# Kernel tuning notes

Hardware: AMD Instinct MI355X
Metric: run time of the kernel (lower is better)

The kernel has to match this reference:

```python
import jax, jax.numpy as jnp
import numpy as np

N_NODES = 10000
N_EDGES = 320000
N_GRAPHS = 64
K = 10
IN_C, HID_C, OUT_C = 128, 256, 128


def setup_inputs() -> dict:
    key = jax.random.key(0)
    ks = jax.random.split(key, 10)
    s_in = 1.0 / np.sqrt(IN_C)
    s_hid = 1.0 / np.sqrt(HID_C)
    return {
        "x": jax.random.normal(ks[0], (N_NODES, IN_C), jnp.float32),
        "W0": jax.random.normal(ks[1], (K, IN_C, HID_C), jnp.float32) * s_in,
        "b0": jnp.zeros((HID_C,), jnp.float32),
        "W1": jax.random.normal(ks[2], (K, HID_C, HID_C), jnp.float32) * s_hid,
        "b1": jnp.zeros((HID_C,), jnp.float32),
        "W2": jax.random.normal(ks[3], (K, HID_C, HID_C), jnp.float32) * s_hid,
        "b2": jnp.zeros((HID_C,), jnp.float32),
        "W_out": jax.random.normal(ks[4], (HID_C, OUT_C), jnp.float32) * s_hid,
        "b_out": jnp.zeros((OUT_C,), jnp.float32),
        "edge_index": jax.random.randint(ks[5], (2, N_EDGES), 0, N_NODES, jnp.int64),
        "batch": jnp.sort(jax.random.randint(ks[6], (N_NODES,), 0, N_GRAPHS, jnp.int64)),
    }


def _edge_norm(src, dst, n):
    # Scaled Laplacian L_hat = 2L/lambda_max - I with lambda_max=2 and sym norm
    # => L_hat = -D^{-1/2} A D^{-1/2} (diagonal entries cancel to 0).
    deg = jnp.zeros((n,), jnp.float32).at[src].add(1.0)
    dis = jnp.where(deg > 0, jax.lax.rsqrt(jnp.maximum(deg, 1.0)), 0.0)
    return -dis[src] * dis[dst]


def _propagate(x, src, dst, w, n):
    # message = w * x[src], aggregated by sum at dst
    return jax.ops.segment_sum(w[:, None] * x[src], dst, num_segments=n)


def _cheb_conv(x, src, dst, w, W, b, n):
    # Tx_0 = x; Tx_1 = L_hat x; Tx_k = 2 L_hat Tx_{k-1} - Tx_{k-2}
    K_ = W.shape[0]
    Tx0 = x
    out = Tx0 @ W[0]
    Tx1 = _propagate(Tx0, src, dst, w, n)
    out = out + Tx1 @ W[1]
    for k in range(2, K_):
        Tx2 = 2.0 * _propagate(Tx1, src, dst, w, n) - Tx0
        out = out + Tx2 @ W[k]
        Tx0, Tx1 = Tx1, Tx2
    return out + b


def reference(x, W0, b0, W1, b1, W2, b2, W_out, b_out, edge_index, batch):
    n = x.shape[0]
    src, dst = edge_index[0], edge_index[1]
    w = _edge_norm(src, dst, n)
    # 3 ChebConv layers, each followed by ReLU (norm=None, dropout=0)
    h = jax.nn.relu(_cheb_conv(x, src, dst, w, W0, b0, n))
    h = jax.nn.relu(_cheb_conv(h, src, dst, w, W1, b1, n))
    h = jax.nn.relu(_cheb_conv(h, src, dst, w, W2, b2, n))
    # global_mean_pool over batch ids
    sums = jax.ops.segment_sum(h, batch, num_segments=N_GRAPHS)
    cnts = jax.ops.segment_sum(jnp.ones((n,), h.dtype), batch, num_segments=N_GRAPHS)
    pooled = sums / jnp.maximum(cnts, 1.0)[:, None]
    return pooled @ W_out + b_out
```

## Files before the change

### kernel.cpp

```cpp
#include <hip/hip_runtime.h>
#include <cstdint>
#include <cstddef>

#define N_NODES 10000
#define N_EDGES 320000
#define N_GRAPHS 64
#define KCHEB 10
#define C_IN 128
#define C_HID 256
#define C_OUTC 128
#define POOL_CHUNK 40

static inline size_t align_up(size_t v, size_t a){ return (v + a - 1) / a * a; }

typedef __attribute__((ext_vector_type(8))) _Float16 half8;
typedef __attribute__((ext_vector_type(2))) _Float16 h2;
typedef __attribute__((ext_vector_type(4))) float f32x4;


__global__ void k_deg(const int* __restrict__ src, const int* __restrict__ dst,
                      int* __restrict__ deg, int* __restrict__ indeg){
  int e = blockIdx.x*blockDim.x + threadIdx.x;
  if(e < N_EDGES){
    atomicAdd(&deg[src[e]], 1);
    atomicAdd(&indeg[dst[e]], 1);
  }
}

__global__ __launch_bounds__(1024) void k_scan(const int* __restrict__ cnt,
                                               int* __restrict__ offs,
                                               int* __restrict__ cursor,
                                               const int* __restrict__ deg,
                                               float* __restrict__ dis,
                                               int* __restrict__ perm){
  __shared__ int part[1024];
  __shared__ int hist[256];
  __shared__ int hoff[256];
  const int n = N_NODES;
  const int CH = (n + 1023) / 1024;
  int tid = threadIdx.x;
  int base = tid * CH;
  if(tid < 256) hist[tid] = 0;
  int s = 0;
  for(int i = 0; i < CH; i++){
    int idx = base + i;
    if(idx < n){
      s += cnt[idx];
      int d = deg[idx];
      dis[idx] = d > 0 ? rsqrtf((float)d) : 0.f;
    }
  }
  part[tid] = s;
  __syncthreads();
  for(int off = 1; off < 1024; off <<= 1){
    int v = (tid >= off) ? part[tid - off] : 0;
    __syncthreads();
    part[tid] += v;
    __syncthreads();
  }
  int run = (tid == 0) ? 0 : part[tid - 1];
  for(int i = 0; i < CH; i++){
    int idx = base + i;
    if(idx < n){
      offs[idx] = run;
      cursor[idx] = run;
      run += cnt[idx];
      int d = cnt[idx]; if(d > 255) d = 255;
      atomicAdd(&hist[d], 1);
    }
  }
  if(tid == 1023) offs[n] = part[1023];
  __syncthreads();
  if(tid == 0){
    int r2 = 0;
    for(int d = 255; d >= 0; d--){ hoff[d] = r2; r2 += hist[d]; }
  }
  __syncthreads();
  for(int i = 0; i < CH; i++){
    int idx = base + i;
    if(idx < n){
      int d = cnt[idx]; if(d > 255) d = 255;
      int p0 = atomicAdd(&hoff[d], 1);
      perm[p0] = idx;
    }
  }
}

__global__ void k_scatter(const int* __restrict__ src, const int* __restrict__ dst,
                          const float* __restrict__ dis, int* __restrict__ cursor,
                          int* __restrict__ csr_s, unsigned* __restrict__ csr_wp){
  int e = blockIdx.x*blockDim.x + threadIdx.x;
  if(e < N_EDGES){
    int s = src[e], d = dst[e];
    float w = -dis[s] * dis[d];
    unsigned short wb = __builtin_bit_cast(unsigned short, (_Float16)w);
    int p = atomicAdd(&cursor[d], 1);
    csr_s[p] = s;
    csr_wp[p] = (unsigned)wb * 0x00010001u;
  }
}

__global__ __launch_bounds__(128) void k_gbounds(const int* __restrict__ batch,
                                                 int* __restrict__ gstart,
                                                 int* __restrict__ gcnt){
  int g = threadIdx.x;
  if(g <= N_GRAPHS){
    int lo = 0, hi = N_NODES;
    while(lo < hi){
      int mid = (lo + hi) >> 1;
      if(batch[mid] < g) lo = mid + 1; else hi = mid;
    }
    gstart[g] = lo;
  }
  __syncthreads();
  if(g < N_GRAPHS) gcnt[g] = gstart[g + 1] - gstart[g];
}


__device__ inline void hfma4(h2* a, uint4 v, unsigned wbits){
  h2 w2 = __builtin_bit_cast(h2, wbits);
  a[0] += __builtin_bit_cast(h2, v.x) * w2;
  a[1] += __builtin_bit_cast(h2, v.y) * w2;
  a[2] += __builtin_bit_cast(h2, v.z) * w2;
  a[3] += __builtin_bit_cast(h2, v.w) * w2;
}

__global__ __launch_bounds__(256) void k_prop256h(const _Float16* __restrict__ Xb,
                                                  const _Float16* __restrict__ Pb,
                                                  _Float16* __restrict__ tx,
                                                  const int* __restrict__ csr_s,
                                                  const unsigned* __restrict__ csr_wp,
                                                  const int* __restrict__ offs,
                                                  const int* __restrict__ perm,
                                                  float alpha){
  const int stride  = KCHEB * C_HID;
  const int strideB = stride * 2;
  int bid  = blockIdx.x;
  int half = (bid >> 2) & 1;
  int lh   = (bid >> 3) * 4 + (bid & 3);
  int l15  = threadIdx.x & 15;
  int lane = threadIdx.x & 63;
  int b16  = lane & 48;
  int e8   = l15 & 7;
  int nidx = lh * 16 + (threadIdx.x >> 4);
  if(nidx >= N_NODES) return;
  int node = perm[nidx];
  int j0 = offs[node], j1 = offs[node + 1];
  h2 a[4] = {};
  const char* __restrict__ gbase = (const char*)Xb + (half * (C_HID/2) + l15 * 8) * 2;
  int j = j0;
  int sv = 0; unsigned wv = 0;
  bool have = (j + 7 < j1);
  if(have){ sv = csr_s[j + e8] * strideB; wv = csr_wp[j + e8]; }
  while(have){
    int jn = j + 8;
    bool more = (jn + 7 < j1);
    int sv2 = 0; unsigned wv2 = 0;
    if(more){ sv2 = csr_s[jn + e8] * strideB; wv2 = csr_wp[jn + e8]; }
    uint4 v[8];
#pragma unroll
    for(int i = 0; i < 8; i++){
      int si = __shfl(sv, b16 + i);
      v[i] = *(const uint4*)(gbase + si);
    }
#pragma unroll
    for(int i = 0; i < 8; i++){
      unsigned wi = (unsigned)__shfl((int)wv, b16 + i);
      hfma4(a, v[i], wi);
    }
    sv = sv2; wv = wv2; j = jn; have = more;
  }
  for(; j < j1; j++){
    int si = csr_s[j] * strideB;
    uint4 v0 = *(const uint4*)(gbase + si);
    hfma4(a, v0, csr_wp[j]);
  }
  _Float16 ah = (_Float16)alpha;
  h2 al = {ah, ah};
  h2 r[4];
#pragma unroll
  for(int i = 0; i < 4; i++) r[i] = a[i] * al;
  size_t off = (size_t)node * stride + half * (C_HID/2) + l15 * 8;
  if(Pb){
    uint4 pv = *(const uint4*)(Pb + off);
    r[0] -= __builtin_bit_cast(h2, pv.x);
    r[1] -= __builtin_bit_cast(h2, pv.y);
    r[2] -= __builtin_bit_cast(h2, pv.z);
    r[3] -= __builtin_bit_cast(h2, pv.w);
  }
  uint4 ob;
  ob.x = __builtin_bit_cast(unsigned, r[0]);
  ob.y = __builtin_bit_cast(unsigned, r[1]);
  ob.z = __builtin_bit_cast(unsigned, r[2]);
  ob.w = __builtin_bit_cast(unsigned, r[3]);
  *(uint4*)(tx + off) = ob;
}

__global__ __launch_bounds__(256) void k_prop128(const _Float16* __restrict__ Xb,
                                                 const _Float16* __restrict__ Pb,
                                                 _Float16* __restrict__ tx,
                                                 const int* __restrict__ csr_s,
                                                 const unsigned* __restrict__ csr_wp,
                                                 const int* __restrict__ offs,
                                                 const int* __restrict__ perm,
                                                 float alpha){
  const int stride  = KCHEB * C_IN;
  const int strideB = stride * 2;
  int hl   = threadIdx.x & 31;
  int b32  = threadIdx.x & 32;
  int e8   = hl & 7;
  int node = perm[blockIdx.x * 8 + (threadIdx.x >> 5)];
  int j0 = offs[node], j1 = offs[node + 1];
  h2 a[2] = {};
  const char* __restrict__ gbase = (const char*)Xb + hl * 8;
  int j = j0;
  int sv = 0; unsigned wv = 0;
  bool have = (j + 7 < j1);
  if(have){ sv = csr_s[j + e8] * strideB; wv = csr_wp[j + e8]; }
  while(have){
    int jn = j + 8;
    bool more = (jn + 7 < j1);
    int sv2 = 0; unsigned wv2 = 0;
    if(more){ sv2 = csr_s[jn + e8] * strideB; wv2 = csr_wp[jn + e8]; }
    uint2 v[8];
#pragma unroll
    for(int i = 0; i < 8; i++){
      int si = __shfl(sv, b32 + i);
      v[i] = *(const uint2*)(gbase + si);
    }
#pragma unroll
    for(int i = 0; i < 8; i++){
      unsigned wi = (unsigned)__shfl((int)wv, b32 + i);
      h2 w2 = __builtin_bit_cast(h2, wi);
      a[0] += __builtin_bit_cast(h2, v[i].x) * w2;
      a[1] += __builtin_bit_cast(h2, v[i].y) * w2;
    }
    sv = sv2; wv = wv2; j = jn; have = more;
  }
  for(; j < j1; j++){
    int si = csr_s[j] * strideB;
    h2 w2 = __builtin_bit_cast(h2, csr_wp[j]);
    uint2 v0 = *(const uint2*)(gbase + si);
    a[0] += __builtin_bit_cast(h2, v0.x) * w2;
    a[1] += __builtin_bit_cast(h2, v0.y) * w2;
  }
  _Float16 ah = (_Float16)alpha;
  h2 al = {ah, ah};
  h2 r0 = a[0] * al, r1 = a[1] * al;
  size_t off = (size_t)node * stride + hl * 4;
  if(Pb){
    uint2 pv = *(const uint2*)(Pb + off);
    r0 -= __builtin_bit_cast(h2, pv.x);
    r1 -= __builtin_bit_cast(h2, pv.y);
  }
  uint2 ob;
  ob.x = __builtin_bit_cast(unsigned, r0);
  ob.y = __builtin_bit_cast(unsigned, r1);
  *(uint2*)(tx + off) = ob;
}

template<int C>
__global__ void k_f2h(const float* __restrict__ X, _Float16* __restrict__ tx,
                      int tx_stride){
  int idx = blockIdx.x * blockDim.x + threadIdx.x;
  const int GPR = C / 4;
  if(idx < N_NODES * GPR){
    int r = idx / GPR;
    int c = (idx - r * GPR) * 4;
    float4 v = *(const float4*)(X + (size_t)r * C + c);
    h2 p0 = {(_Float16)v.x, (_Float16)v.y};
    h2 p1 = {(_Float16)v.z, (_Float16)v.w};
    uint2 ob;
    ob.x = __builtin_bit_cast(unsigned, p0);
    ob.y = __builtin_bit_cast(unsigned, p1);
    *(uint2*)(tx + (size_t)r * tx_stride + c) = ob;
  }
}

__global__ __launch_bounds__(256) void k_wt3t(const float* __restrict__ W0, _Float16* __restrict__ WT0,
                                              const float* __restrict__ W1, _Float16* __restrict__ WT1,
                                              const float* __restrict__ W2, _Float16* __restrict__ WT2){
  __shared__ float t[32][33];
  int b = blockIdx.x;
  const float* W; _Float16* WT; int R; int tb;
  if(b < 320){ W = W0; WT = WT0; R = 1280; tb = b; }
  else if(b < 960){ W = W1; WT = WT1; R = 2560; tb = b - 320; }
  else { W = W2; WT = WT2; R = 2560; tb = b - 960; }
  int tr = tb >> 3, tc = tb & 7;
  int tx = threadIdx.x & 31, ty = threadIdx.x >> 5;
#pragma unroll
  for(int i = 0; i < 4; i++){
    int r = tr * 32 + ty + 8 * i;
    t[ty + 8 * i][tx] = W[(size_t)r * 256 + tc * 32 + tx];
  }
  __syncthreads();
#pragma unroll
  for(int i = 0; i < 4; i++){
    int o = tc * 32 + ty + 8 * i;
    WT[(size_t)o * R + tr * 32 + tx] = (_Float16)t[tx][ty + 8 * i];
  }
}


__global__ __launch_bounds__(256) void k_gemm_f(const _Float16* __restrict__ A,
                                                const _Float16* __restrict__ BT,
                                                const float* __restrict__ bias,
                                                float* __restrict__ H,
                                                _Float16* __restrict__ tx2,
                                                int M, int Ktot){
  int b = blockIdx.x;
  int xcd = b & 7;
  int l = b >> 3;
  int m = xcd + 8 * (l >> 2);
  int n = l & 3;
  if(m * 64 >= M) return;
  int row0 = m * 64, col0 = n * 64;

  __shared__ short As[2][64 * 64];
  __shared__ short Bs[2][64 * 64];
  int tid = threadIdx.x;
  int lane = tid & 63;
  int wave = tid >> 6;
  int l15 = lane & 15;
  int quad = lane >> 4;
  int wm = (wave & 1) * 32;
  int wn = (wave >> 1) * 32;

  int e0 = tid, e1 = tid + 256;
  int r0 = e0 >> 3, g0 = e0 & 7;
  int r1 = e1 >> 3, g1 = e1 & 7;
  int gr0 = row0 + r0, gr1 = row0 + r1;
  int sa0 = r0 * 64 + ((g0 ^ (r0 & 7)) * 8);
  int sa1 = r1 * 64 + ((g1 ^ (r1 & 7)) * 8);

  f32x4 acc[2][2] = {};
  uint4 av0, av1, bv0, bv1;

  auto load = [&](int k0){
    av0 = (gr0 < M) ? *(const uint4*)(A + (size_t)gr0 * Ktot + k0 + g0 * 8)
                    : make_uint4(0u, 0u, 0u, 0u);
    av1 = (gr1 < M) ? *(const uint4*)(A + (size_t)gr1 * Ktot + k0 + g1 * 8)
                    : make_uint4(0u, 0u, 0u, 0u);
    bv0 = *(const uint4*)(BT + (size_t)(col0 + r0) * Ktot + k0 + g0 * 8);
    bv1 = *(const uint4*)(BT + (size_t)(col0 + r1) * Ktot + k0 + g1 * 8);
  };
  auto stor = [&](int buf){
    *(uint4*)(&As[buf][sa0]) = av0;
    *(uint4*)(&As[buf][sa1]) = av1;
    *(uint4*)(&Bs[buf][sa0]) = bv0;
    *(uint4*)(&Bs[buf][sa1]) = bv1;
  };

  load(0);
  stor(0);
  __syncthreads();
  int nk = Ktot >> 6;
  for(int it = 0; it < nk; it++){
    int cur = it & 1;
    if(it + 1 < nk) load((it + 1) << 6);
#pragma unroll
    for(int kk = 0; kk < 64; kk += 32){
      int g = (kk >> 3) + quad;
      half8 a[2], bb[2];
#pragma unroll
      for(int mi = 0; mi < 2; mi++){
        int r = wm + mi * 16 + l15;
        a[mi] = *(const half8*)(&As[cur][r * 64 + ((g ^ (r & 7)) * 8)]);
      }
#pragma unroll
      for(int ni = 0; ni < 2; ni++){
        int nn = wn + ni * 16 + l15;
        bb[ni] = *(const half8*)(&Bs[cur][nn * 64 + ((g ^ (nn & 7)) * 8)]);
      }
#pragma unroll
      for(int mi = 0; mi < 2; mi++)
#pragma unroll
        for(int ni = 0; ni < 2; ni++)
          acc[mi][ni] = __builtin_amdgcn_mfma_f32_16x16x32_f16(a[mi], bb[ni], acc[mi][ni], 0, 0, 0);
    }
    if(it + 1 < nk){
      stor(cur ^ 1);
      __syncthreads();
    }
  }

  const int K256 = KCHEB * C_HID;
#pragma unroll
  for(int mi = 0; mi < 2; mi++){
#pragma unroll
    for(int ni = 0; ni < 2; ni++){
      int gcol = col0 + wn + ni * 16 + l15;
      float bv = bias[gcol];
#pragma unroll
      for(int r = 0; r < 4; r++){
        int grow = row0 + wm + mi * 16 + quad * 4 + r;
        if(grow < M){
          float v = fmaxf(acc[mi][ni][r] + bv, 0.f);
          if(tx2) tx2[(size_t)grow * K256 + gcol] = (_Float16)v;
          else    H[(size_t)grow * C_HID + gcol] = v;
        }
      }
    }
  }
}


__global__ __launch_bounds__(256) void k_pool2(const float* __restrict__ h,
                                               const int* __restrict__ batch,
                                               float* __restrict__ gsum){
  int c  = threadIdx.x;
  int n0 = blockIdx.x * POOL_CHUNK;
  int n1 = n0 + POOL_CHUNK;
  if(n1 > N_NODES) n1 = N_NODES;
  if(n0 >= n1) return;
  float acc = 0.f;
  int cur = batch[n0];
  for(int n = n0; n < n1; n++){
    int g = batch[n];
    if(g != cur){
      atomicAdd(&gsum[cur * C_HID + c], acc);
      acc = 0.f;
      cur = g;
    }
    acc += h[(size_t)n * C_HID + c];
  }
  atomicAdd(&gsum[cur * C_HID + c], acc);
}

__global__ __launch_bounds__(128) void k_final(const float* __restrict__ gsum,
                                               const int* __restrict__ gcnt,
                                               const float* __restrict__ Wout,
                                               const float* __restrict__ bout,
                                               float* __restrict__ out){
  int g = blockIdx.x;
  int o = threadIdx.x;
  float inv = 1.f / fmaxf((float)gcnt[g], 1.f);
  float acc = bout[o];
  for(int c = 0; c < C_HID; c++) acc += gsum[g * C_HID + c] * inv * Wout[c * C_OUTC + o];
  out[g * C_OUTC + o] = acc;
}


extern "C" void kernel_launch(void* const* d_in, const int* in_sizes, int n_in,
                              void* d_out, int out_size, void* d_ws, size_t ws_size,
                              hipStream_t stream){
  const float* x    = (const float*)d_in[0];
  const float* W0   = (const float*)d_in[1];
  const float* b0   = (const float*)d_in[2];
  const float* W1   = (const float*)d_in[3];
  const float* b1   = (const float*)d_in[4];
  const float* W2   = (const float*)d_in[5];
  const float* b2   = (const float*)d_in[6];
  const float* Wout = (const float*)d_in[7];
  const float* bout = (const float*)d_in[8];
  const int*   ei   = (const int*)d_in[9];
  const int*   batch= (const int*)d_in[10];
  const int* src = ei;
  const int* dst = ei + N_EDGES;
  float* out = (float*)d_out;

  char* p = (char*)d_ws;
  auto alloc = [&](size_t bytes)->char*{ char* r = p; p += align_up(bytes, 256); return r; };

  int*   deg    = (int*)  alloc(N_NODES * 4);
  int*   indeg  = (int*)  alloc(N_NODES * 4);
  int*   offs   = (int*)  alloc((N_NODES + 1) * 4);
  int*   cursor = (int*)  alloc(N_NODES * 4);
  float* dis    = (float*)alloc(N_NODES * 4);
  int*   perm   = (int*)  alloc(N_NODES * 4);
  int*   csr_s  = (int*)  alloc(N_EDGES * 4);
  unsigned* csr_wp = (unsigned*)alloc(N_EDGES * 4);
  int*   gcnt   = (int*)  alloc(N_GRAPHS * 4);
  int*   gstart = (int*)  alloc((N_GRAPHS + 1) * 4);
  float* gsum   = (float*)alloc(N_GRAPHS * C_HID * 4);

  const size_t txBytes = (size_t)N_NODES * (KCHEB * C_HID) * 2;
  _Float16* txP = (_Float16*)alloc(txBytes);
  _Float16* txQ = (_Float16*)alloc(txBytes);
  _Float16* WT0 = (_Float16*)alloc((size_t)KCHEB * C_IN  * C_HID * 2);
  _Float16* WT1 = (_Float16*)alloc((size_t)KCHEB * C_HID * C_HID * 2);
  _Float16* WT2 = (_Float16*)alloc((size_t)KCHEB * C_HID * C_HID * 2);
  float* Hb = (float*)alloc((size_t)N_NODES * C_HID * 4);

  hipMemsetAsync(deg,   0, N_NODES * 4, stream);
  hipMemsetAsync(indeg, 0, N_NODES * 4, stream);
  hipMemsetAsync(gsum,  0, N_GRAPHS * C_HID * 4, stream);

  const int TB = 256;
  int egrid = (N_EDGES + TB - 1) / TB;

  k_deg<<<egrid, TB, 0, stream>>>(src, dst, deg, indeg);
  k_scan<<<1, 1024, 0, stream>>>(indeg, offs, cursor, deg, dis, perm);
  k_scatter<<<egrid, TB, 0, stream>>>(src, dst, dis, cursor, csr_s, csr_wp);
  k_gbounds<<<1, 128, 0, stream>>>(batch, gstart, gcnt);
  k_wt3t<<<1600, 256, 0, stream>>>(W0, WT0, W1, WT1, W2, WT2);

  const int K128 = KCHEB * C_IN;
  const int K256 = KCHEB * C_HID;
  const int GEMM_BLOCKS = 640;
  const int PROP_H_BLOCKS = 1256;
  const int PROP_1_BLOCKS = N_NODES / 8;

  {
    int ng = N_NODES * (C_IN / 4);
    k_f2h<C_IN><<<(ng + TB - 1) / TB, TB, 0, stream>>>(x, txP, K128);
    for(int k = 1; k < KCHEB; k++){
      const _Float16* Xb = txP + (size_t)(k - 1) * C_IN;
      const _Float16* Pb = (k >= 2) ? txP + (size_t)(k - 2) * C_IN : nullptr;
      _Float16* tx = txP + (size_t)k * C_IN;
      k_prop128<<<PROP_1_BLOCKS, 256, 0, stream>>>(Xb, Pb, tx, csr_s, csr_wp, offs, perm,
                                                   k == 1 ? 1.f : 2.f);
    }
    k_gemm_f<<<GEMM_BLOCKS, 256, 0, stream>>>(txP, WT0, b0, nullptr, txQ, N_NODES, K128);
  }

  {
    for(int k = 1; k < KCHEB; k++){
      const _Float16* Xb = txQ + (size_t)(k - 1) * C_HID;
      const _Float16* Pb = (k >= 2) ? txQ + (size_t)(k - 2) * C_HID : nullptr;
      _Float16* tx = txQ + (size_t)k * C_HID;
      k_prop256h<<<PROP_H_BLOCKS, 256, 0, stream>>>(Xb, Pb, tx, csr_s, csr_wp, offs, perm,
                                                    k == 1 ? 1.f : 2.f);
    }
    k_gemm_f<<<GEMM_BLOCKS, 256, 0, stream>>>(txQ, WT1, b1, nullptr, txP, N_NODES, K256);
  }

  {
    for(int k = 1; k < KCHEB; k++){
      const _Float16* Xb = txP + (size_t)(k - 1) * C_HID;
      const _Float16* Pb = (k >= 2) ? txP + (size_t)(k - 2) * C_HID : nullptr;
      _Float16* tx = txP + (size_t)k * C_HID;
      k_prop256h<<<PROP_H_BLOCKS, 256, 0, stream>>>(Xb, Pb, tx, csr_s, csr_wp, offs, perm,
                                                    k == 1 ? 1.f : 2.f);
    }
    k_gemm_f<<<GEMM_BLOCKS, 256, 0, stream>>>(txP, WT2, b2, Hb, nullptr, N_NODES, K256);
  }

  k_pool2<<<(N_NODES + POOL_CHUNK - 1) / POOL_CHUNK, 256, 0, stream>>>(Hb, batch, gsum);
  k_final<<<N_GRAPHS, C_OUTC, 0, stream>>>(gsum, gcnt, Wout, bout, out);
}
```

Measured before the change: 626.8 us.

## Fuse mean-pool into last GEMM epilogue and merge small setup kernels

The final GEMM now stages its ReLU output tile in shared memory and accumulates per-graph column sums directly with atomics. This removes the fp32 H buffer write/read and the separate pooling kernel. Graph-boundary search moves into the scan kernel, and the x-to-half conversion is merged into the weight transpose kernel, cutting launch count. Atomic contention per GEMM block may increase slightly.

```diff
diff --git a/kernel.cpp b/kernel.cpp
--- a/kernel.cpp
+++ b/kernel.cpp
@@ -9,7 +9,6 @@
 #define C_IN 128
 #define C_HID 256
 #define C_OUTC 128
-#define POOL_CHUNK 40
 
 static inline size_t align_up(size_t v, size_t a){ return (v + a - 1) / a * a; }
 
@@ -32,7 +31,10 @@
                                                int* __restrict__ cursor,
                                                const int* __restrict__ deg,
                                                float* __restrict__ dis,
-                                               int* __restrict__ perm){
+                                               int* __restrict__ perm,
+                                               const int* __restrict__ batch,
+                                               int* __restrict__ gstart,
+                                               int* __restrict__ gcnt){
   __shared__ int part[1024];
   __shared__ int hist[256];
   __shared__ int hoff[256];
@@ -41,6 +43,14 @@
   int tid = threadIdx.x;
   int base = tid * CH;
   if(tid < 256) hist[tid] = 0;
+  if(tid <= N_GRAPHS){
+    int lo = 0, hi = N_NODES;
+    while(lo < hi){
+      int mid = (lo + hi) >> 1;
+      if(batch[mid] < tid) lo = mid + 1; else hi = mid;
+    }
+    gstart[tid] = lo;
+  }
   int s = 0;
   for(int i = 0; i < CH; i++){
     int idx = base + i;
@@ -52,6 +62,7 @@
   }
   part[tid] = s;
   __syncthreads();
+  if(tid < N_GRAPHS) gcnt[tid] = gstart[tid + 1] - gstart[tid];
   for(int off = 1; off < 1024; off <<= 1){
     int v = (tid >= off) ? part[tid - off] : 0;
     __syncthreads();
@@ -98,22 +109,6 @@
     csr_s[p] = s;
     csr_wp[p] = (unsigned)wb * 0x00010001u;
   }
-}
-
-__global__ __launch_bounds__(128) void k_gbounds(const int* __restrict__ batch,
-                                                 int* __restrict__ gstart,
-                                                 int* __restrict__ gcnt){
-  int g = threadIdx.x;
-  if(g <= N_GRAPHS){
-    int lo = 0, hi = N_NODES;
-    while(lo < hi){
-      int mid = (lo + hi) >> 1;
-      if(batch[mid] < g) lo = mid + 1; else hi = mid;
-    }
-    gstart[g] = lo;
-  }
-  __syncthreads();
-  if(g < N_GRAPHS) gcnt[g] = gstart[g + 1] - gstart[g];
 }
 
 
@@ -259,29 +254,27 @@
   *(uint2*)(tx + off) = ob;
 }
 
-template<int C>
-__global__ void k_f2h(const float* __restrict__ X, _Float16* __restrict__ tx,
-                      int tx_stride){
-  int idx = blockIdx.x * blockDim.x + threadIdx.x;
-  const int GPR = C / 4;
-  if(idx < N_NODES * GPR){
-    int r = idx / GPR;
-    int c = (idx - r * GPR) * 4;
-    float4 v = *(const float4*)(X + (size_t)r * C + c);
-    h2 p0 = {(_Float16)v.x, (_Float16)v.y};
-    h2 p1 = {(_Float16)v.z, (_Float16)v.w};
-    uint2 ob;
-    ob.x = __builtin_bit_cast(unsigned, p0);
-    ob.y = __builtin_bit_cast(unsigned, p1);
-    *(uint2*)(tx + (size_t)r * tx_stride + c) = ob;
-  }
-}
-
-__global__ __launch_bounds__(256) void k_wt3t(const float* __restrict__ W0, _Float16* __restrict__ WT0,
+__global__ __launch_bounds__(256) void k_prep(const float* __restrict__ W0, _Float16* __restrict__ WT0,
                                               const float* __restrict__ W1, _Float16* __restrict__ WT1,
-                                              const float* __restrict__ W2, _Float16* __restrict__ WT2){
+                                              const float* __restrict__ W2, _Float16* __restrict__ WT2,
+                                              const float* __restrict__ X, _Float16* __restrict__ txP){
+  int b = blockIdx.x;
+  if(b >= 1600){
+    int idx = (b - 1600) * 256 + threadIdx.x;
+    if(idx < N_NODES * (C_IN / 4)){
+      int r = idx >> 5;
+      int c = (idx & 31) * 4;
+      float4 v = *(const float4*)(X + (size_t)r * C_IN + c);
+      h2 p0 = {(_Float16)v.x, (_Float16)v.y};
+      h2 p1 = {(_Float16)v.z, (_Float16)v.w};
+      uint2 ob;
+      ob.x = __builtin_bit_cast(unsigned, p0);
+      ob.y = __builtin_bit_cast(unsigned, p1);
+      *(uint2*)(txP + (size_t)r * (KCHEB * C_IN) + c) = ob;
+    }
+    return;
+  }
   __shared__ float t[32][33];
-  int b = blockIdx.x;
   const float* W; _Float16* WT; int R; int tb;
   if(b < 320){ W = W0; WT = WT0; R = 1280; tb = b; }
   else if(b < 960){ W = W1; WT = WT1; R = 2560; tb = b - 320; }
@@ -305,8 +298,9 @@
 __global__ __launch_bounds__(256) void k_gemm_f(const _Float16* __restrict__ A,
                                                 const _Float16* __restrict__ BT,
                                                 const float* __restrict__ bias,
-                                                float* __restrict__ H,
                                                 _Float16* __restrict__ tx2,
+                                                const int* __restrict__ batch,
+                                                float* __restrict__ gsum,
                                                 int M, int Ktot){
   int b = blockIdx.x;
   int xcd = b & 7;
@@ -384,48 +378,60 @@
     }
   }
 
-  const int K256 = KCHEB * C_HID;
-#pragma unroll
-  for(int mi = 0; mi < 2; mi++){
-#pragma unroll
-    for(int ni = 0; ni < 2; ni++){
-      int gcol = col0 + wn + ni * 16 + l15;
-      float bv = bias[gcol];
-#pragma unroll
-      for(int r = 0; r < 4; r++){
-        int grow = row0 + wm + mi * 16 + quad * 4 + r;
-        if(grow < M){
-          float v = fmaxf(acc[mi][ni][r] + bv, 0.f);
-          if(tx2) tx2[(size_t)grow * K256 + gcol] = (_Float16)v;
-          else    H[(size_t)grow * C_HID + gcol] = v;
+  if(tx2){
+    const int K256 = KCHEB * C_HID;
+#pragma unroll
+    for(int mi = 0; mi < 2; mi++){
+#pragma unroll
+      for(int ni = 0; ni < 2; ni++){
+        int gcol = col0 + wn + ni * 16 + l15;
+        float bv = bias[gcol];
+#pragma unroll
+        for(int r = 0; r < 4; r++){
+          int grow = row0 + wm + mi * 16 + quad * 4 + r;
+          if(grow < M){
+            float v = fmaxf(acc[mi][ni][r] + bv, 0.f);
+            tx2[(size_t)grow * K256 + gcol] = (_Float16)v;
+          }
         }
       }
     }
-  }
-}
-
-
-__global__ __launch_bounds__(256) void k_pool2(const float* __restrict__ h,
-                                               const int* __restrict__ batch,
-                                               float* __restrict__ gsum){
-  int c  = threadIdx.x;
-  int n0 = blockIdx.x * POOL_CHUNK;
-  int n1 = n0 + POOL_CHUNK;
-  if(n1 > N_NODES) n1 = N_NODES;
-  if(n0 >= n1) return;
-  float acc = 0.f;
-  int cur = batch[n0];
-  for(int n = n0; n < n1; n++){
-    int g = batch[n];
-    if(g != cur){
-      atomicAdd(&gsum[cur * C_HID + c], acc);
-      acc = 0.f;
-      cur = g;
-    }
-    acc += h[(size_t)n * C_HID + c];
-  }
-  atomicAdd(&gsum[cur * C_HID + c], acc);
-}
+  } else {
+    __syncthreads();
+    float* Ls = (float*)As;
+#pragma unroll
+    for(int mi = 0; mi < 2; mi++){
+#pragma unroll
+      for(int ni = 0; ni < 2; ni++){
+        int lc = wn + ni * 16 + l15;
+        float bv = bias[col0 + lc];
+#pragma unroll
+        for(int r = 0; r < 4; r++){
+          int lr = wm + mi * 16 + quad * 4 + r;
+          Ls[lr * 64 + lc] = fmaxf(acc[mi][ni][r] + bv, 0.f);
+        }
+      }
+    }
+    __syncthreads();
+    int col  = tid & 63;
+    int rseg = tid >> 6;
+    int rb   = rseg * 16;
+    float accp = 0.f;
+    int curg = -1;
+    for(int rr = 0; rr < 16; rr++){
+      int grow = row0 + rb + rr;
+      if(grow >= M) break;
+      int g = batch[grow];
+      if(g != curg){
+        if(curg >= 0) atomicAdd(&gsum[curg * C_HID + col0 + col], accp);
+        accp = 0.f; curg = g;
+      }
+      accp += Ls[(rb + rr) * 64 + col];
+    }
+    if(curg >= 0) atomicAdd(&gsum[curg * C_HID + col0 + col], accp);
+  }
+}
+
 
 __global__ __launch_bounds__(128) void k_final(const float* __restrict__ gsum,
                                                const int* __restrict__ gcnt,
@@ -480,7 +486,6 @@
   _Float16* WT0 = (_Float16*)alloc((size_t)KCHEB * C_IN  * C_HID * 2);
   _Float16* WT1 = (_Float16*)alloc((size_t)KCHEB * C_HID * C_HID * 2);
   _Float16* WT2 = (_Float16*)alloc((size_t)KCHEB * C_HID * C_HID * 2);
-  float* Hb = (float*)alloc((size_t)N_NODES * C_HID * 4);
 
   hipMemsetAsync(deg,   0, N_NODES * 4, stream);
   hipMemsetAsync(indeg, 0, N_NODES * 4, stream);
@@ -490,10 +495,9 @@
   int egrid = (N_EDGES + TB - 1) / TB;
 
   k_deg<<<egrid, TB, 0, stream>>>(src, dst, deg, indeg);
-  k_scan<<<1, 1024, 0, stream>>>(indeg, offs, cursor, deg, dis, perm);
+  k_scan<<<1, 1024, 0, stream>>>(indeg, offs, cursor, deg, dis, perm, batch, gstart, gcnt);
   k_scatter<<<egrid, TB, 0, stream>>>(src, dst, dis, cursor, csr_s, csr_wp);
-  k_gbounds<<<1, 128, 0, stream>>>(batch, gstart, gcnt);
-  k_wt3t<<<1600, 256, 0, stream>>>(W0, WT0, W1, WT1, W2, WT2);
+  k_prep<<<2850, 256, 0, stream>>>(W0, WT0, W1, WT1, W2, WT2, x, txP);
 
   const int K128 = KCHEB * C_IN;
   const int K256 = KCHEB * C_HID;
@@ -502,8 +506,6 @@
   const int PROP_1_BLOCKS = N_NODES / 8;
 
   {
-    int ng = N_NODES * (C_IN / 4);
-    k_f2h<C_IN><<<(ng + TB - 1) / TB, TB, 0, stream>>>(x, txP, K128);
     for(int k = 1; k < KCHEB; k++){
       const _Float16* Xb = txP + (size_t)(k - 1) * C_IN;
       const _Float16* Pb = (k >= 2) ? txP + (size_t)(k - 2) * C_IN : nullptr;
@@ -511,7 +513,8 @@
       k_prop128<<<PROP_1_BLOCKS, 256, 0, stream>>>(Xb, Pb, tx, csr_s, csr_wp, offs, perm,
                                                    k == 1 ? 1.f : 2.f);
     }
-    k_gemm_f<<<GEMM_BLOCKS, 256, 0, stream>>>(txP, WT0, b0, nullptr, txQ, N_NODES, K128);
+    k_gemm_f<<<GEMM_BLOCKS, 256, 0, stream>>>(txP, WT0, b0, txQ, nullptr, nullptr,
+                                              N_NODES, K128);
   }
 
   {
@@ -522,7 +525,8 @@
       k_prop256h<<<PROP_H_BLOCKS, 256, 0, stream>>>(Xb, Pb, tx, csr_s, csr_wp, offs, perm,
                                                     k == 1 ? 1.f : 2.f);
     }
-    k_gemm_f<<<GEMM_BLOCKS, 256, 0, stream>>>(txQ, WT1, b1, nullptr, txP, N_NODES, K256);
+    k_gemm_f<<<GEMM_BLOCKS, 256, 0, stream>>>(txQ, WT1, b1, txP, nullptr, nullptr,
+                                              N_NODES, K256);
   }
 
   {
@@ -533,9 +537,9 @@
       k_prop256h<<<PROP_H_BLOCKS, 256, 0, stream>>>(Xb, Pb, tx, csr_s, csr_wp, offs, perm,
                                                     k == 1 ? 1.f : 2.f);
     }
-    k_gemm_f<<<GEMM_BLOCKS, 256, 0, stream>>>(txP, WT2, b2, Hb, nullptr, N_NODES, K256);
-  }
-
-  k_pool2<<<(N_NODES + POOL_CHUNK - 1) / POOL_CHUNK, 256, 0, stream>>>(Hb, batch, gsum);
+    k_gemm_f<<<GEMM_BLOCKS, 256, 0, stream>>>(txP, WT2, b2, nullptr, batch, gsum,
+                                              N_NODES, K256);
+  }
+
   k_final<<<N_GRAPHS, C_OUTC, 0, stream>>>(gsum, gcnt, Wout, bout, out);
 }
```

Measured after the change: 614.0 us (median of 2 runs). 1.02x faster.
